# Kernel optimization log

Hardware: AMD Instinct MI355X
Metric: run time of the kernel (lower is better)

The kernel has to match this reference:

```python
import jax, jax.numpy as jnp
import numpy as np

H = 12  # num_heads

def _attn(q, k, v):
    # q,k,v: [B,H,N,D]; SDPA default scale 1/sqrt(D)
    D = q.shape[-1]
    scores = jnp.einsum('bhnd,bhmd->bhnm', q, k) / jnp.sqrt(jnp.asarray(D, q.dtype))
    p = jax.nn.softmax(scores, axis=-1)
    return jnp.einsum('bhnm,bhmd->bhnd', p, v)

def setup_inputs() -> dict:
    key = jax.random.key(0)
    ks = jax.random.split(key, 5)
    B, N, C = 2, 2048, 768
    s = 0.02
    return {
        'x': jax.random.normal(ks[0], (B, N, C), jnp.float32),
        'Wq': jax.random.normal(ks[1], (C, 2 * C), jnp.float32) * s,
        'Wk': jax.random.normal(ks[2], (C, 2 * C), jnp.float32) * s,
        'Wv': jax.random.normal(ks[3], (C, C), jnp.float32) * s,
        'lambda_p': jnp.zeros((H, 1, 1), jnp.float32),
        'Wo': jax.random.normal(ks[4], (C, C), jnp.float32) * s,
        'bo': jnp.zeros((C,), jnp.float32),
    }

def reference(x, Wq, Wk, Wv, lambda_p, Wo, bo):
    B, N, C = x.shape
    D = C // H
    # [B,N,2C] -> [2,B,H,N,D]
    q = (x @ Wq).reshape(B, N, 2, H, D).transpose(2, 0, 3, 1, 4)
    k = (x @ Wk).reshape(B, N, 2, H, D).transpose(2, 0, 3, 1, 4)
    v = (x @ Wv).reshape(B, N, H, D).transpose(0, 2, 1, 3)
    out1 = _attn(q[0], k[0], v)
    out2 = _attn(q[1], k[1], v)
    lam = jnp.exp(lambda_p)  # [H,1,1] broadcasts over [B,H,N,D]
    out = out1 - lam * out2
    out = out.transpose(0, 2, 1, 3).reshape(B, N, C)
    return out @ Wo + bo
```

## Files before the change

### kernel.cpp

```cpp
#include <hip/hip_runtime.h>

typedef unsigned short u16;
typedef unsigned int u32;
typedef unsigned long long u64;
typedef __bf16 bf16x8 __attribute__((ext_vector_type(8)));
typedef float f32x4 __attribute__((ext_vector_type(4)));
typedef float f32x16 __attribute__((ext_vector_type(16)));

#define B_ 2
#define N_ 2048
#define C_ 768
#define H_ 12
#define M_ 4096
#define SCALE_LOG2 0.18033688011112042f

#define KSTR 136
#define PSTR 72
#define K1OFF 8704
#define VOFF 17408
#define POFF 26112
#define PWSZ 2304

static __device__ __forceinline__ u16 f2bf(float f) {
  u32 u = __builtin_bit_cast(u32, f);
  u32 r = u + 0x7fffu + ((u >> 16) & 1u);
  return (u16)(r >> 16);
}
static __device__ __forceinline__ float fexp2(float x) {
#if __has_builtin(__builtin_amdgcn_exp2f)
  return __builtin_amdgcn_exp2f(x);
#else
  return __expf(x * 0.6931471805599453f);
#endif
}
static __device__ __forceinline__ u32 pack_bf16(float a, float b) {
  u32 r;
  asm("v_cvt_pk_bf16_f32 %0, %1, %2" : "=v"(r) : "v"(a), "v"(b));
  return r;
}
static __device__ __forceinline__ bf16x8 mk8(uint2 a, uint2 b) {
  uint4 u = make_uint4(a.x, a.y, b.x, b.y);
  return __builtin_bit_cast(bf16x8, u);
}

static __device__ __forceinline__ void gload16(const void* g, void* lds_base) {
  __builtin_amdgcn_global_load_lds(
      (__attribute__((address_space(1))) void*)(u64)(g),
      (__attribute__((address_space(3))) void*)(u32)(u64)(lds_base), 16, 0, 0);
}

__global__ __launch_bounds__(256) void k_cvt4(const float* __restrict__ x,
                                              u16* __restrict__ xb, int n4) {
  int i = blockIdx.x * 256 + threadIdx.x;
  if (i >= n4) return;
  float4 v = ((const float4*)x)[i];
  ushort4 o;
  o.x = f2bf(v.x); o.y = f2bf(v.y); o.z = f2bf(v.z); o.w = f2bf(v.w);
  ((ushort4*)xb)[i] = o;
}

__global__ __launch_bounds__(256) void k_tconv2(const float* __restrict__ W0,
                                                const float* __restrict__ W1,
                                                u16* __restrict__ Wt, int K, int N) {
  const float* W = blockIdx.z ? W1 : W0;
  u16* dst = Wt + (u64)blockIdx.z * N * K;
  __shared__ float t[32][33];
  int n0 = blockIdx.x * 32, k0 = blockIdx.y * 32;
  int tx = threadIdx.x, ty = threadIdx.y;
#pragma unroll
  for (int i = 0; i < 4; i++)
    t[ty + i * 8][tx] = W[(u64)(k0 + ty + i * 8) * N + n0 + tx];
  __syncthreads();
#pragma unroll
  for (int i = 0; i < 4; i++)
    dst[(u64)(n0 + ty + i * 8) * K + k0 + tx] = f2bf(t[tx][ty + i * 8]);
}

__global__ __launch_bounds__(256) void k_gemm_qkv(const u16* __restrict__ A,
                                                  const u16* __restrict__ WQK,
                                                  const u16* __restrict__ WV,
                                                  u16* __restrict__ QKb,
                                                  u16* __restrict__ Vtout) {
  __shared__ u16 As[128 * 32];
  __shared__ u16 Bs[128 * 32];
  const int t = threadIdx.x;
  const int w = t >> 6, l = t & 63;
  const int wr = w >> 1, wc = w & 1;
  const int la = l & 15, lg = l >> 4;
  const int srow = l >> 2, scb = (l & 3) << 4;
  const int by = blockIdx.y;
  const bool isV = by >= 24;

  f32x4 acc[4][4];
#pragma unroll
  for (int i = 0; i < 4; i++)
#pragma unroll
    for (int j = 0; j < 4; j++) acc[i][j] = f32x4{0.f, 0.f, 0.f, 0.f};

  const u16* Ag = A + (u64)(blockIdx.x * 128) * 768;
  const u16* Bg = isV ? WV + (u64)((by - 24) * 128) * 768 : WQK + (u64)(by * 128) * 768;

  for (int k0 = 0; k0 < 768; k0 += 32) {
#pragma unroll
    for (int j = 0; j < 2; j++) {
      int r = (w * 2 + j) * 16 + srow;
      gload16((const char*)(Ag + (u64)r * 768 + k0) + scb, (char*)As + (w * 2 + j) * 1024);
      gload16((const char*)(Bg + (u64)r * 768 + k0) + scb, (char*)Bs + (w * 2 + j) * 1024);
    }
    __syncthreads();
    bf16x8 af[4], bfr[4];
#pragma unroll
    for (int m = 0; m < 4; m++)
      af[m] = *(const bf16x8*)(As + (wr * 64 + m * 16 + la) * 32 + lg * 8);
#pragma unroll
    for (int n = 0; n < 4; n++)
      bfr[n] = *(const bf16x8*)(Bs + (wc * 64 + n * 16 + la) * 32 + lg * 8);
#pragma unroll
    for (int m = 0; m < 4; m++)
#pragma unroll
      for (int n = 0; n < 4; n++)
        acc[m][n] =
            __builtin_amdgcn_mfma_f32_16x16x32_bf16(af[m], bfr[n], acc[m][n], 0, 0, 0);
    __syncthreads();
  }

#pragma unroll
  for (int m = 0; m < 4; m++) {
#pragma unroll
    for (int n = 0; n < 4; n++) {
      int grow0 = blockIdx.x * 128 + wr * 64 + m * 16 + lg * 4;
      if (!isV) {
        int gcol = by * 128 + wc * 64 + n * 16 + la;
        float sc = (gcol < 1536) ? SCALE_LOG2 : 1.0f;
#pragma unroll
        for (int j = 0; j < 4; j++)
          QKb[(u64)(grow0 + j) * 3072 + gcol] = f2bf(acc[m][n][j] * sc);
      } else {
        int gcol = (by - 24) * 128 + wc * 64 + n * 16 + la;
        ushort4 o;
        o.x = f2bf(acc[m][n][0]); o.y = f2bf(acc[m][n][1]);
        o.z = f2bf(acc[m][n][2]); o.w = f2bf(acc[m][n][3]);
        *(ushort4*)(Vtout + (u64)gcol * M_ + grow0) = o;
      }
    }
  }
}

__global__ __launch_bounds__(256) void k_gemm_out(const u16* __restrict__ A,
                                                  const u16* __restrict__ Bt,
                                                  float* __restrict__ Cout,
                                                  const float* __restrict__ bias) {
  __shared__ u16 As[128 * 32];
  __shared__ u16 Bs[128 * 32];
  const int t = threadIdx.x;
  const int w = t >> 6, l = t & 63;
  const int wr = w >> 1, wc = w & 1;
  const int la = l & 15, lg = l >> 4;
  const int srow = l >> 2, scb = (l & 3) << 4;

  f32x4 acc[4][4];
#pragma unroll
  for (int i = 0; i < 4; i++)
#pragma unroll
    for (int j = 0; j < 4; j++) acc[i][j] = f32x4{0.f, 0.f, 0.f, 0.f};

  const u16* Ag = A + (u64)(blockIdx.x * 128) * 768;
  const u16* Bg = Bt + (u64)(blockIdx.y * 128) * 768;

  for (int k0 = 0; k0 < 768; k0 += 32) {
#pragma unroll
    for (int j = 0; j < 2; j++) {
      int r = (w * 2 + j) * 16 + srow;
      gload16((const char*)(Ag + (u64)r * 768 + k0) + scb, (char*)As + (w * 2 + j) * 1024);
      gload16((const char*)(Bg + (u64)r * 768 + k0) + scb, (char*)Bs + (w * 2 + j) * 1024);
    }
    __syncthreads();
    bf16x8 af[4], bfr[4];
#pragma unroll
    for (int m = 0; m < 4; m++)
      af[m] = *(const bf16x8*)(As + (wr * 64 + m * 16 + la) * 32 + lg * 8);
#pragma unroll
    for (int n = 0; n < 4; n++)
      bfr[n] = *(const bf16x8*)(Bs + (wc * 64 + n * 16 + la) * 32 + lg * 8);
#pragma unroll
    for (int m = 0; m < 4; m++)
#pragma unroll
      for (int n = 0; n < 4; n++)
        acc[m][n] =
            __builtin_amdgcn_mfma_f32_16x16x32_bf16(af[m], bfr[n], acc[m][n], 0, 0, 0);
    __syncthreads();
  }

#pragma unroll
  for (int m = 0; m < 4; m++) {
#pragma unroll
    for (int n = 0; n < 4; n++) {
      int grow0 = blockIdx.x * 128 + wr * 64 + m * 16 + lg * 4;
      int gcol = blockIdx.y * 128 + wc * 64 + n * 16 + la;
      float bb = bias[gcol];
#pragma unroll
      for (int j = 0; j < 4; j++)
        Cout[(u64)(grow0 + j) * 768 + gcol] = acc[m][n][j] + bb;
    }
  }
}

__global__ __launch_bounds__(256, 2) void k_attn7(const u16* __restrict__ QKb,
                                                  const u16* __restrict__ Vt,
                                                  const float* __restrict__ lamp,
                                                  u16* __restrict__ Ob) {
  const int hw = blockIdx.x;
  const int wid = (hw & 7) * 96 + (hw >> 3);
  const int qt = wid & 31;
  const int hb = wid >> 5;
  const int h = hb % H_, b = hb / H_;

  __shared__ __align__(16) char smem[35328];
  const int t = threadIdx.x, w = t >> 6, l = t & 63;
  const int p = w >> 1, kvh = w & 1;
  const int ql = l & 31, hh = l >> 5;

  bf16x8 qf[2][4];
#pragma unroll
  for (int s = 0; s < 2; s++) {
    const u16* qrow =
        QKb + (u64)(b * N_ + qt * 64 + s * 32 + ql) * 3072 + p * 768 + h * 64 + hh * 8;
#pragma unroll
    for (int c = 0; c < 4; c++) qf[s][c] = *(const bf16x8*)(qrow + 16 * c);
  }

  f32x16 oacc[2][2];
#pragma unroll
  for (int s = 0; s < 2; s++)
#pragma unroll
    for (int dh = 0; dh < 2; dh++)
#pragma unroll
      for (int r = 0; r < 16; r++) oacc[s][dh][r] = 0.f;
  float l_run[2] = {0.f, 0.f};

  const int rA = t >> 3, cb = (t & 7) << 4;
  const char* kg = (const char*)(QKb + (u64)(b * N_ + rA) * 3072 + 1536 + h * 64) + cb;
  const char* vg = (const char*)(Vt + (u64)(h * 64 + rA) * M_ + b * N_) + cb;
  const u64 KR32 = (u64)32 * 3072 * 2;
  const u64 VR32 = (u64)32 * M_ * 2;
  const u64 KSTEP = (u64)64 * 3072 * 2;
  char* d0a = smem + rA * KSTR + cb;
  char* d0b = smem + (rA + 32) * KSTR + cb;

  uint4 rk0A, rk0B, rk1A, rk1B, rvA, rvB;
#define LOADS6()                              \
  do {                                        \
    rk0A = *(const uint4*)(kg);               \
    rk0B = *(const uint4*)(kg + KR32);        \
    rk1A = *(const uint4*)(kg + 1536);        \
    rk1B = *(const uint4*)(kg + 1536 + KR32); \
    rvA = *(const uint4*)(vg);                \
    rvB = *(const uint4*)(vg + VR32);         \
  } while (0)
  LOADS6();

  const char* kbase = smem + p * K1OFF + (32 * kvh + ql) * KSTR + 16 * hh;
  const char* vb0 = smem + VOFF + ql * KSTR + 64 * kvh + 16 * hh;
  const char* vb1 = smem + VOFF + (32 + ql) * KSTR + 64 * kvh + 16 * hh;
  char* pb = smem + POFF + w * PWSZ;
  char* pwr = pb + ql * PSTR + 8 * hh;
  const char* prd = pb + ql * PSTR + 16 * hh;

  for (int kt = 0; kt < 32; kt++) {
    asm volatile("s_waitcnt vmcnt(0)" ::: "memory");
    __builtin_amdgcn_sched_barrier(0);
    *(uint2*)(d0a) = make_uint2(rk0A.x, rk0A.y);
    *(uint2*)(d0a + 8) = make_uint2(rk0A.z, rk0A.w);
    *(uint2*)(d0b) = make_uint2(rk0B.x, rk0B.y);
    *(uint2*)(d0b + 8) = make_uint2(rk0B.z, rk0B.w);
    *(uint2*)(d0a + K1OFF) = make_uint2(rk1A.x, rk1A.y);
    *(uint2*)(d0a + K1OFF + 8) = make_uint2(rk1A.z, rk1A.w);
    *(uint2*)(d0b + K1OFF) = make_uint2(rk1B.x, rk1B.y);
    *(uint2*)(d0b + K1OFF + 8) = make_uint2(rk1B.z, rk1B.w);
    *(uint2*)(d0a + VOFF) = make_uint2(rvA.x, rvA.y);
    *(uint2*)(d0a + VOFF + 8) = make_uint2(rvA.z, rvA.w);
    *(uint2*)(d0b + VOFF) = make_uint2(rvB.x, rvB.y);
    *(uint2*)(d0b + VOFF + 8) = make_uint2(rvB.z, rvB.w);
    asm volatile("s_waitcnt lgkmcnt(0)" ::: "memory");
    __builtin_amdgcn_s_barrier();
    kg += KSTEP;
    vg += 128;
    if (kt < 31) LOADS6();
    __builtin_amdgcn_sched_barrier(0);

    bf16x8 kf[4];
#pragma unroll
    for (int c = 0; c < 4; c++)
      kf[c] = mk8(*(const uint2*)(kbase + 32 * c), *(const uint2*)(kbase + 32 * c + 8));
    bf16x8 vf[2][2];
#pragma unroll
    for (int dh = 0; dh < 2; dh++) {
      const char* vb = dh ? vb1 : vb0;
#pragma unroll
      for (int c2 = 0; c2 < 2; c2++)
        vf[dh][c2] =
            mk8(*(const uint2*)(vb + 32 * c2), *(const uint2*)(vb + 32 * c2 + 8));
    }

#pragma unroll
    for (int s = 0; s < 2; s++) {
      f32x16 st;
#pragma unroll
      for (int r = 0; r < 16; r++) st[r] = 0.f;
      __builtin_amdgcn_s_setprio(1);
#pragma unroll
      for (int c = 0; c < 4; c++)
        st = __builtin_amdgcn_mfma_f32_32x32x16_bf16(kf[c], qf[s][c], st, 0, 0, 0);
      __builtin_amdgcn_s_setprio(0);

      float sm[16];
#pragma unroll
      for (int r = 0; r < 16; r++) {
        st[r] = fexp2(st[r]);
        sm[r] = st[r];
      }
#pragma unroll
      for (int sd = 8; sd >= 1; sd >>= 1)
#pragma unroll
        for (int r = 0; r < sd; r++) sm[r] += sm[r + sd];
      l_run[s] += sm[0] + __shfl_xor(sm[0], 32, 64);

#pragma unroll
      for (int g = 0; g < 4; g++) {
        uint2 pk;
        pk.x = pack_bf16(st[4 * g + 0], st[4 * g + 1]);
        pk.y = pack_bf16(st[4 * g + 2], st[4 * g + 3]);
        *(uint2*)(pwr + 16 * g) = pk;
      }
      bf16x8 pa[2];
#pragma unroll
      for (int c2 = 0; c2 < 2; c2++)
        pa[c2] =
            mk8(*(const uint2*)(prd + 32 * c2), *(const uint2*)(prd + 32 * c2 + 8));

      __builtin_amdgcn_s_setprio(1);
#pragma unroll
      for (int c2 = 0; c2 < 2; c2++)
#pragma unroll
        for (int dh = 0; dh < 2; dh++)
          oacc[s][dh] = __builtin_amdgcn_mfma_f32_32x32x16_bf16(pa[c2], vf[dh][c2],
                                                                oacc[s][dh], 0, 0, 0);
      __builtin_amdgcn_s_setprio(0);
    }
    __builtin_amdgcn_s_barrier();
  }

  float* Os = (float*)smem;
  float* lsc = (float*)(smem + 32768);
  __syncthreads();
  if (kvh == 1) {
#pragma unroll
    for (int s = 0; s < 2; s++) {
#pragma unroll
      for (int dh = 0; dh < 2; dh++)
#pragma unroll
        for (int r = 0; r < 16; r++) {
          int q = s * 32 + (r & 3) + 8 * (r >> 2) + 4 * hh;
          Os[(p * 64 + q) * 64 + dh * 32 + ql] = oacc[s][dh][r];
        }
      lsc[p * 64 + s * 32 + ql] = l_run[s];
    }
  }
  __syncthreads();
  if (kvh == 0) {
#pragma unroll
    for (int s = 0; s < 2; s++) {
#pragma unroll
      for (int dh = 0; dh < 2; dh++)
#pragma unroll
        for (int r = 0; r < 16; r++) {
          int q = s * 32 + (r & 3) + 8 * (r >> 2) + 4 * hh;
          oacc[s][dh][r] += Os[(p * 64 + q) * 64 + dh * 32 + ql];
        }
      l_run[s] += lsc[p * 64 + s * 32 + ql];
    }
  }
  __syncthreads();
  if (kvh == 0 && p == 1) {
    float lam = __expf(lamp[h]);
    float inv[2] = {lam / l_run[0], lam / l_run[1]};
#pragma unroll
    for (int s = 0; s < 2; s++)
#pragma unroll
      for (int dh = 0; dh < 2; dh++)
#pragma unroll
        for (int r = 0; r < 16; r++) {
          int qm = (r & 3) + 8 * (r >> 2) + 4 * hh;
          float iT = __shfl(inv[s], qm, 64);
          Os[(64 + s * 32 + qm) * 64 + dh * 32 + ql] = oacc[s][dh][r] * iT;
        }
  }
  __syncthreads();
  if (kvh == 0 && p == 0) {
    float inv[2] = {1.f / l_run[0], 1.f / l_run[1]};
    u16* Og = Ob + (u64)(b * N_ + qt * 64) * C_ + h * 64;
#pragma unroll
    for (int s = 0; s < 2; s++)
#pragma unroll
      for (int dh = 0; dh < 2; dh++)
#pragma unroll
        for (int r = 0; r < 16; r++) {
          int qm = (r & 3) + 8 * (r >> 2) + 4 * hh;
          float iT = __shfl(inv[s], qm, 64);
          int q = s * 32 + qm, d = dh * 32 + ql;
          float v = oacc[s][dh][r] * iT - Os[(64 + q) * 64 + d];
          Og[(u64)q * C_ + d] = f2bf(v);
        }
  }
}

extern "C" void kernel_launch(void* const* d_in, const int* in_sizes, int n_in,
                              void* d_out, int out_size, void* d_ws, size_t ws_size,
                              hipStream_t stream) {
  const float* x = (const float*)d_in[0];
  const float* Wq = (const float*)d_in[1];
  const float* Wk = (const float*)d_in[2];
  const float* Wv = (const float*)d_in[3];
  const float* lamp = (const float*)d_in[4];
  const float* Wo = (const float*)d_in[5];
  const float* bo = (const float*)d_in[6];

  char* ws = (char*)d_ws;
  u16* xb = (u16*)ws;    ws += (u64)M_ * C_ * 2;
  u16* wqkt = (u16*)ws;  ws += (u64)4 * C_ * C_ * 2;
  u16* wvo = (u16*)ws;   ws += (u64)2 * C_ * C_ * 2;
  u16* QKb = (u16*)ws;   ws += (u64)M_ * 4 * C_ * 2;
  u16* Vt = (u16*)ws;    ws += (u64)C_ * M_ * 2;
  u16* Ob = (u16*)ws;    ws += (u64)M_ * C_ * 2;
  u16* wvt = wvo;
  u16* wot = wvo + (u64)C_ * C_;

  k_cvt4<<<dim3(M_ * C_ / 4 / 256), 256, 0, stream>>>(x, xb, M_ * C_ / 4);
  k_tconv2<<<dim3(48, 24, 2), dim3(32, 8), 0, stream>>>(Wq, Wk, wqkt, 768, 1536);
  k_tconv2<<<dim3(24, 24, 2), dim3(32, 8), 0, stream>>>(Wv, Wo, wvo, 768, 768);
  k_gemm_qkv<<<dim3(32, 30), 256, 0, stream>>>(xb, wqkt, wvt, QKb, Vt);
  k_attn7<<<dim3(768), 256, 0, stream>>>(QKb, Vt, lamp, Ob);
  k_gemm_out<<<dim3(32, 6), 256, 0, stream>>>(Ob, wot, (float*)d_out, bo);
}
```

Baseline: 150.6 us.

## Halve attention query tile to 32 rows and double grid for higher occupancy

```diff
diff --git a/kernel.cpp b/kernel.cpp
--- a/kernel.cpp
+++ b/kernel.cpp
@@ -20,6 +20,7 @@
 #define VOFF 17408
 #define POFF 26112
 #define PWSZ 2304
+#define SMSZ 35328
 
 static __device__ __forceinline__ u16 f2bf(float f) {
   u32 u = __builtin_bit_cast(u32, f);
@@ -205,38 +206,33 @@
   }
 }
 
-__global__ __launch_bounds__(256, 2) void k_attn7(const u16* __restrict__ QKb,
-                                                  const u16* __restrict__ Vt,
-                                                  const float* __restrict__ lamp,
-                                                  u16* __restrict__ Ob) {
+__global__ __launch_bounds__(256, 4) void k_attn11(const u16* __restrict__ QKb,
+                                                   const u16* __restrict__ Vt,
+                                                   const float* __restrict__ lamp,
+                                                   u16* __restrict__ Ob) {
   const int hw = blockIdx.x;
-  const int wid = (hw & 7) * 96 + (hw >> 3);
-  const int qt = wid & 31;
-  const int hb = wid >> 5;
+  const int wid = (hw & 7) * 192 + (hw >> 3);
+  const int qt2 = wid & 63;
+  const int hb = wid >> 6;
   const int h = hb % H_, b = hb / H_;
 
-  __shared__ __align__(16) char smem[35328];
+  __shared__ __align__(16) char smem[SMSZ];
   const int t = threadIdx.x, w = t >> 6, l = t & 63;
   const int p = w >> 1, kvh = w & 1;
   const int ql = l & 31, hh = l >> 5;
 
-  bf16x8 qf[2][4];
-#pragma unroll
-  for (int s = 0; s < 2; s++) {
-    const u16* qrow =
-        QKb + (u64)(b * N_ + qt * 64 + s * 32 + ql) * 3072 + p * 768 + h * 64 + hh * 8;
-#pragma unroll
-    for (int c = 0; c < 4; c++) qf[s][c] = *(const bf16x8*)(qrow + 16 * c);
-  }
-
-  f32x16 oacc[2][2];
-#pragma unroll
-  for (int s = 0; s < 2; s++)
-#pragma unroll
-    for (int dh = 0; dh < 2; dh++)
-#pragma unroll
-      for (int r = 0; r < 16; r++) oacc[s][dh][r] = 0.f;
-  float l_run[2] = {0.f, 0.f};
+  const u16* qrow =
+      QKb + (u64)(b * N_ + qt2 * 32 + ql) * 3072 + p * 768 + h * 64 + hh * 8;
+  bf16x8 qf[4];
+#pragma unroll
+  for (int c = 0; c < 4; c++) qf[c] = *(const bf16x8*)(qrow + 16 * c);
+
+  f32x16 oacc[2];
+#pragma unroll
+  for (int dh = 0; dh < 2; dh++)
+#pragma unroll
+    for (int r = 0; r < 16; r++) oacc[dh][r] = 0.f;
+  float l_run = 0.f;
 
   const int rA = t >> 3, cb = (t & 7) << 4;
   const char* kg = (const char*)(QKb + (u64)(b * N_ + rA) * 3072 + 1536 + h * 64) + cb;
@@ -302,115 +298,101 @@
             mk8(*(const uint2*)(vb + 32 * c2), *(const uint2*)(vb + 32 * c2 + 8));
     }
 
-#pragma unroll
-    for (int s = 0; s < 2; s++) {
-      f32x16 st;
-#pragma unroll
-      for (int r = 0; r < 16; r++) st[r] = 0.f;
-      __builtin_amdgcn_s_setprio(1);
-#pragma unroll
-      for (int c = 0; c < 4; c++)
-        st = __builtin_amdgcn_mfma_f32_32x32x16_bf16(kf[c], qf[s][c], st, 0, 0, 0);
-      __builtin_amdgcn_s_setprio(0);
-
-      float sm[16];
-#pragma unroll
-      for (int r = 0; r < 16; r++) {
-        st[r] = fexp2(st[r]);
-        sm[r] = st[r];
-      }
-#pragma unroll
-      for (int sd = 8; sd >= 1; sd >>= 1)
-#pragma unroll
-        for (int r = 0; r < sd; r++) sm[r] += sm[r + sd];
-      l_run[s] += sm[0] + __shfl_xor(sm[0], 32, 64);
-
-#pragma unroll
-      for (int g = 0; g < 4; g++) {
-        uint2 pk;
-        pk.x = pack_bf16(st[4 * g + 0], st[4 * g + 1]);
-        pk.y = pack_bf16(st[4 * g + 2], st[4 * g + 3]);
-        *(uint2*)(pwr + 16 * g) = pk;
-      }
-      bf16x8 pa[2];
-#pragma unroll
-      for (int c2 = 0; c2 < 2; c2++)
-        pa[c2] =
-            mk8(*(const uint2*)(prd + 32 * c2), *(const uint2*)(prd + 32 * c2 + 8));
-
-      __builtin_amdgcn_s_setprio(1);
-#pragma unroll
-      for (int c2 = 0; c2 < 2; c2++)
-#pragma unroll
-        for (int dh = 0; dh < 2; dh++)
-          oacc[s][dh] = __builtin_amdgcn_mfma_f32_32x32x16_bf16(pa[c2], vf[dh][c2],
-                                                                oacc[s][dh], 0, 0, 0);
-      __builtin_amdgcn_s_setprio(0);
-    }
+    f32x16 st;
+#pragma unroll
+    for (int r = 0; r < 16; r++) st[r] = 0.f;
+    __builtin_amdgcn_s_setprio(1);
+#pragma unroll
+    for (int c = 0; c < 4; c++)
+      st = __builtin_amdgcn_mfma_f32_32x32x16_bf16(kf[c], qf[c], st, 0, 0, 0);
+    __builtin_amdgcn_s_setprio(0);
+
+    float sm[16];
+#pragma unroll
+    for (int r = 0; r < 16; r++) {
+      st[r] = fexp2(st[r]);
+      sm[r] = st[r];
+    }
+#pragma unroll
+    for (int sd = 8; sd >= 1; sd >>= 1)
+#pragma unroll
+      for (int r = 0; r < sd; r++) sm[r] += sm[r + sd];
+    l_run += sm[0] + __shfl_xor(sm[0], 32, 64);
+
+#pragma unroll
+    for (int g = 0; g < 4; g++) {
+      uint2 pk;
+      pk.x = pack_bf16(st[4 * g + 0], st[4 * g + 1]);
+      pk.y = pack_bf16(st[4 * g + 2], st[4 * g + 3]);
+      *(uint2*)(pwr + 16 * g) = pk;
+    }
+    bf16x8 pa[2];
+#pragma unroll
+    for (int c2 = 0; c2 < 2; c2++)
+      pa[c2] = mk8(*(const uint2*)(prd + 32 * c2), *(const uint2*)(prd + 32 * c2 + 8));
+
+    __builtin_amdgcn_s_setprio(1);
+#pragma unroll
+    for (int c2 = 0; c2 < 2; c2++)
+#pragma unroll
+      for (int dh = 0; dh < 2; dh++)
+        oacc[dh] = __builtin_amdgcn_mfma_f32_32x32x16_bf16(pa[c2], vf[dh][c2],
+                                                           oacc[dh], 0, 0, 0);
+    __builtin_amdgcn_s_setprio(0);
     __builtin_amdgcn_s_barrier();
   }
 
   float* Os = (float*)smem;
-  float* lsc = (float*)(smem + 32768);
+  float* lsc = (float*)(smem + 16384);
   __syncthreads();
   if (kvh == 1) {
 #pragma unroll
-    for (int s = 0; s < 2; s++) {
-#pragma unroll
-      for (int dh = 0; dh < 2; dh++)
-#pragma unroll
-        for (int r = 0; r < 16; r++) {
-          int q = s * 32 + (r & 3) + 8 * (r >> 2) + 4 * hh;
-          Os[(p * 64 + q) * 64 + dh * 32 + ql] = oacc[s][dh][r];
-        }
-      lsc[p * 64 + s * 32 + ql] = l_run[s];
-    }
+    for (int dh = 0; dh < 2; dh++)
+#pragma unroll
+      for (int r = 0; r < 16; r++) {
+        int qm = (r & 3) + 8 * (r >> 2) + 4 * hh;
+        Os[(p * 32 + qm) * 64 + dh * 32 + ql] = oacc[dh][r];
+      }
+    lsc[p * 32 + ql] = l_run;
   }
   __syncthreads();
   if (kvh == 0) {
 #pragma unroll
-    for (int s = 0; s < 2; s++) {
-#pragma unroll
-      for (int dh = 0; dh < 2; dh++)
-#pragma unroll
-        for (int r = 0; r < 16; r++) {
-          int q = s * 32 + (r & 3) + 8 * (r >> 2) + 4 * hh;
-          oacc[s][dh][r] += Os[(p * 64 + q) * 64 + dh * 32 + ql];
-        }
-      l_run[s] += lsc[p * 64 + s * 32 + ql];
-    }
+    for (int dh = 0; dh < 2; dh++)
+#pragma unroll
+      for (int r = 0; r < 16; r++) {
+        int qm = (r & 3) + 8 * (r >> 2) + 4 * hh;
+        oacc[dh][r] += Os[(p * 32 + qm) * 64 + dh * 32 + ql];
+      }
+    l_run += lsc[p * 32 + ql];
   }
   __syncthreads();
   if (kvh == 0 && p == 1) {
     float lam = __expf(lamp[h]);
-    float inv[2] = {lam / l_run[0], lam / l_run[1]};
-#pragma unroll
-    for (int s = 0; s < 2; s++)
-#pragma unroll
-      for (int dh = 0; dh < 2; dh++)
-#pragma unroll
-        for (int r = 0; r < 16; r++) {
-          int qm = (r & 3) + 8 * (r >> 2) + 4 * hh;
-          float iT = __shfl(inv[s], qm, 64);
-          Os[(64 + s * 32 + qm) * 64 + dh * 32 + ql] = oacc[s][dh][r] * iT;
-        }
+    float inv = lam / l_run;
+#pragma unroll
+    for (int dh = 0; dh < 2; dh++)
+#pragma unroll
+      for (int r = 0; r < 16; r++) {
+        int qm = (r & 3) + 8 * (r >> 2) + 4 * hh;
+        float iT = __shfl(inv, qm, 64);
+        Os[(32 + qm) * 64 + dh * 32 + ql] = oacc[dh][r] * iT;
+      }
   }
   __syncthreads();
   if (kvh == 0 && p == 0) {
-    float inv[2] = {1.f / l_run[0], 1.f / l_run[1]};
-    u16* Og = Ob + (u64)(b * N_ + qt * 64) * C_ + h * 64;
-#pragma unroll
-    for (int s = 0; s < 2; s++)
-#pragma unroll
-      for (int dh = 0; dh < 2; dh++)
-#pragma unroll
-        for (int r = 0; r < 16; r++) {
-          int qm = (r & 3) + 8 * (r >> 2) + 4 * hh;
-          float iT = __shfl(inv[s], qm, 64);
-          int q = s * 32 + qm, d = dh * 32 + ql;
-          float v = oacc[s][dh][r] * iT - Os[(64 + q) * 64 + d];
-          Og[(u64)q * C_ + d] = f2bf(v);
-        }
+    float inv = 1.f / l_run;
+    u16* Og = Ob + (u64)(b * N_ + qt2 * 32) * C_ + h * 64;
+#pragma unroll
+    for (int dh = 0; dh < 2; dh++)
+#pragma unroll
+      for (int r = 0; r < 16; r++) {
+        int qm = (r & 3) + 8 * (r >> 2) + 4 * hh;
+        float iT = __shfl(inv, qm, 64);
+        int d = dh * 32 + ql;
+        float v = oacc[dh][r] * iT - Os[(32 + qm) * 64 + d];
+        Og[(u64)qm * C_ + d] = f2bf(v);
+      }
   }
 }
 
@@ -439,6 +421,6 @@
   k_tconv2<<<dim3(48, 24, 2), dim3(32, 8), 0, stream>>>(Wq, Wk, wqkt, 768, 1536);
   k_tconv2<<<dim3(24, 24, 2), dim3(32, 8), 0, stream>>>(Wv, Wo, wvo, 768, 768);
   k_gemm_qkv<<<dim3(32, 30), 256, 0, stream>>>(xb, wqkt, wvt, QKb, Vt);
-  k_attn7<<<dim3(768), 256, 0, stream>>>(QKb, Vt, lamp, Ob);
+  k_attn11<<<dim3(1536), 256, 0, stream>>>(QKb, Vt, lamp, Ob);
   k_gemm_out<<<dim3(32, 6), 256, 0, stream>>>(Ob, wot, (float*)d_out, bo);
 }
```

Result: slower. 181.2 us (+20.3%).
